# Kernel optimization log

Measured on AMD Instinct MI355X. Metric: run time of the kernel, lower is better.

The kernel has to match this reference:

```python
import math
from itertools import combinations
import jax, jax.numpy as jnp
import numpy as np

SEQ_LEN = 8
D_IN = 2048
D_OUT = 1152
TSS = 3          # temporal_set_size
WAY = 5
SHOT = 5
N_SUPPORT = WAY * SHOT
N_Q = 100
PE_SCALE = 0.1
LN_EPS = 1e-5

TUPLES = np.array(list(combinations(range(SEQ_LEN), TSS)), dtype=np.int32)  # [56, 3]
T_LEN = TUPLES.shape[0]  # 56


def _positional_encoding(seq_len, d):
    pos = np.arange(seq_len, dtype=np.float32)[:, None]
    div = np.exp(np.arange(0, d, 2, dtype=np.float32) * -(math.log(10000.0) / d))
    pe = np.zeros((seq_len, d), dtype=np.float32)
    pe[:, 0::2] = np.sin(pos * div) * PE_SCALE
    pe[:, 1::2] = np.cos(pos * div) * PE_SCALE
    return jnp.asarray(pe)


def _layernorm(x, g, b):
    mu = jnp.mean(x, axis=-1, keepdims=True)
    var = jnp.mean((x - mu) ** 2, axis=-1, keepdims=True)
    return (x - mu) * jax.lax.rsqrt(var + LN_EPS) * g + b


def setup_inputs() -> dict:
    key = jax.random.key(0)
    ks = jax.random.split(key, 6)
    support_set = jax.random.normal(ks[0], (N_SUPPORT, SEQ_LEN, D_IN), dtype=jnp.float32)
    queries = jax.random.normal(ks[1], (N_Q, SEQ_LEN, D_IN), dtype=jnp.float32)
    # sorted episode layout: class c occupies rows [c*SHOT, (c+1)*SHOT)
    support_labels = jnp.repeat(jnp.arange(WAY, dtype=jnp.int64), SHOT)
    d_flat = TSS * D_IN  # 6144
    k_w = jax.random.normal(ks[2], (d_flat, D_OUT), dtype=jnp.float32) * 0.02
    k_b = jnp.zeros((D_OUT,), dtype=jnp.float32)
    v_w = jax.random.normal(ks[3], (d_flat, D_OUT), dtype=jnp.float32) * 0.02
    v_b = jnp.zeros((D_OUT,), dtype=jnp.float32)
    ln_g = jnp.ones((D_OUT,), dtype=jnp.float32)
    ln_b = jnp.zeros((D_OUT,), dtype=jnp.float32)
    return {"support_set": support_set, "queries": queries,
            "support_labels": support_labels,
            "k_w": k_w, "k_b": k_b, "v_w": v_w, "v_b": v_b,
            "ln_g": ln_g, "ln_b": ln_b}


def reference(support_set, queries, support_labels, k_w, k_b, v_w, v_b, ln_g, ln_b):
    pe = _positional_encoding(SEQ_LEN, D_IN)  # dropout is identity in eval mode
    s = support_set + pe
    q = queries + pe

    def tuplify(x):  # [N, S, D] -> [N, T_LEN, TSS*D]
        return x[:, TUPLES, :].reshape(x.shape[0], T_LEN, TSS * D_IN)

    s_t = tuplify(s)
    q_t = tuplify(q)

    sk = _layernorm(s_t @ k_w + k_b, ln_g, ln_b)  # [25, 56, 1152]
    qk = _layernorm(q_t @ k_w + k_b, ln_g, ln_b)  # [100, 56, 1152]
    sv = s_t @ v_w + v_b                           # [25, 56, 1152]
    qv = q_t @ v_w + v_b                           # [100, 56, 1152]

    scale = 1.0 / math.sqrt(D_OUT)
    dists = []
    align = None
    for c in range(WAY):  # fixed small class loop; class rows are a static slice
        class_k = sk[c * SHOT:(c + 1) * SHOT]  # [SHOT, 56, 1152]
        class_v = sv[c * SHOT:(c + 1) * SHOT]
        # scores: [Q, T, K, T] == torch permute(0,2,1,3) of [Q, K, T, T]
        scores = jnp.einsum('qtd,ksd->qtks', qk, class_k) * scale
        flat = scores.reshape(N_Q, T_LEN, SHOT * T_LEN)
        sm = jax.nn.softmax(flat, axis=-1)
        sm = sm.reshape(N_Q, T_LEN, SHOT, T_LEN).transpose(0, 2, 1, 3)  # [Q, K, T, T]
        align = sm.sum(axis=1)  # [Q, T, T]
        proto = jnp.einsum('qkts,ksd->qtd', sm, class_v)  # [Q, 56, 1152]
        diff = qv - proto
        dists.append(-jnp.sum(diff * diff, axis=(-2, -1)) / T_LEN)  # [Q]
    logits = jnp.stack(dists, axis=1)  # [Q, WAY]
    return logits, align
```

## Files before the change

kernel.cpp:

```cpp
#include <hip/hip_runtime.h>
#include <hip/hip_bf16.h>
#include <math.h>

#define SEQ_LEN 8
#define D_IN 2048
#define D_OUT 1152
#define WAY 5
#define SHOT 5
#define N_SUPPORT 25
#define N_Q 100
#define N_SEQ 125
#define N_ROWS 1000
#define T_LEN 56
#define KS_LEN 280
#define KS_PAD 288
#define NCOLS 6912
#define MQT 5600
#define DPC 9

typedef __attribute__((ext_vector_type(4))) float f32x4;
typedef __attribute__((ext_vector_type(8))) short bf16x8;

__constant__ int TUP[T_LEN][3] = {
  {0,1,2},{0,1,3},{0,1,4},{0,1,5},{0,1,6},{0,1,7},{0,2,3},{0,2,4},{0,2,5},{0,2,6},
  {0,2,7},{0,3,4},{0,3,5},{0,3,6},{0,3,7},{0,4,5},{0,4,6},{0,4,7},{0,5,6},{0,5,7},
  {0,6,7},{1,2,3},{1,2,4},{1,2,5},{1,2,6},{1,2,7},{1,3,4},{1,3,5},{1,3,6},{1,3,7},
  {1,4,5},{1,4,6},{1,4,7},{1,5,6},{1,5,7},{1,6,7},{2,3,4},{2,3,5},{2,3,6},{2,3,7},
  {2,4,5},{2,4,6},{2,4,7},{2,5,6},{2,5,7},{2,6,7},{3,4,5},{3,4,6},{3,4,7},{3,5,6},
  {3,5,7},{3,6,7},{4,5,6},{4,5,7},{4,6,7},{5,6,7}
};

__device__ __forceinline__ ushort f2bf(float f) {
  union { float f; unsigned u; } v; v.f = f;
  unsigned r = v.u + 0x7FFFu + ((v.u >> 16) & 1u);
  return (ushort)(r >> 16);
}
__device__ __forceinline__ float bf2f(ushort u) {
  union { unsigned u; float f; } v; v.u = ((unsigned)u) << 16;
  return v.f;
}
__device__ __forceinline__ void gload16(const void* g, const void* l) {
  __builtin_amdgcn_global_load_lds(
      (const __attribute__((address_space(1))) unsigned int*)g,
      (__attribute__((address_space(3))) unsigned int*)l, 16, 0, 0);
}
template<int N> __device__ __forceinline__ void vmw() {
  asm volatile("s_waitcnt vmcnt(%0)" :: "n"(N) : "memory");
}

__global__ __launch_bounds__(256) void pe_add(const float* __restrict__ sup,
                                              const float* __restrict__ que,
                                              ushort* __restrict__ X) {
  int idx = blockIdx.x * 256 + threadIdx.x;
  if (idx >= N_ROWS * D_IN) return;
  int d = idx & (D_IN - 1);
  int r = idx >> 11;
  int i = r & 7;
  int h2 = d & ~1;
  float freq = expf((float)h2 * (-9.210340371976184f / (float)D_IN));
  float ang = (float)i * freq;
  float pe = ((d & 1) ? cosf(ang) : sinf(ang)) * 0.1f;
  float src = (r < N_SUPPORT * SEQ_LEN) ? sup[idx] : que[idx - N_SUPPORT * SEQ_LEN * D_IN];
  X[idx] = f2bf(src + pe);
}

__global__ __launch_bounds__(256) void wtrans(const float* __restrict__ kw,
                                              const float* __restrict__ vw,
                                              ushort* __restrict__ WT) {
  __shared__ float tile[64][65];
  int bx = blockIdx.x;
  int by = blockIdx.y;
  int b = bx / 18;
  int n0 = (bx % 18) * 64;
  int k0 = by * 64;
  const float* src = ((b & 1) ? vw : kw) + (size_t)(b >> 1) * D_IN * D_OUT;
  int tid = threadIdx.x;
#pragma unroll
  for (int it = 0; it < 4; ++it) {
    int lin4 = it * 256 + tid;
    int kk = lin4 >> 4;
    int n4 = (lin4 & 15) * 4;
    float4 v = *(const float4*)(src + (size_t)(k0 + kk) * D_OUT + n0 + n4);
    tile[kk][n4 + 0] = v.x; tile[kk][n4 + 1] = v.y;
    tile[kk][n4 + 2] = v.z; tile[kk][n4 + 3] = v.w;
  }
  __syncthreads();
#pragma unroll
  for (int it = 0; it < 4; ++it) {
    int lin = it * 1024 + tid * 4;
    int nn = lin >> 6, kk = lin & 63;
    ushort4 o;
    o.x = f2bf(tile[kk + 0][nn]); o.y = f2bf(tile[kk + 1][nn]);
    o.z = f2bf(tile[kk + 2][nn]); o.w = f2bf(tile[kk + 3][nn]);
    *(ushort4*)&WT[((size_t)(b * D_OUT + n0 + nn)) * D_IN + k0 + kk] = o;
  }
}

template<int EPI, int NT>
__global__ __launch_bounds__(256) void gemm_bt(
    const ushort* __restrict__ A, const ushort* __restrict__ BT,
    float* __restrict__ C,
    int M, int N, int K, int lda, int ldb, int ldc, float alpha,
    long batchA, long batchB, long batchC) {
  constexpr int JF = NT / 32;
  constexpr int NCH = 8 + NT / 16;
  __shared__ ushort As[2][128][32];
  __shared__ ushort Bs[2][NT][32];
  int z = blockIdx.z;
  A  += (size_t)z * batchA;
  BT += (size_t)z * batchB;
  C  += (size_t)z * batchC;

  int tid = threadIdx.x;
  int wid = tid >> 6, lane = tid & 63;
  int l16 = lane & 15, lk = lane >> 4;
  int wr = wid >> 1, wc = wid & 1;
  int row0 = blockIdx.x * 128, col0 = blockIdx.y * NT;
  int lrow = lane >> 2;
  int lcol = ((lane & 3) ^ ((lane >> 3) & 3)) * 8;
  int rslot = (lk ^ ((l16 >> 1) & 3)) * 8;

  auto stage = [&](int buf, int t) {
    int k0 = t * 32;
    for (int c = wid; c < NCH; c += 4) {
      if (c < 8) {
        int grow = row0 + c * 16 + lrow;
        grow = grow < M ? grow : M - 1;
        gload16(A + (size_t)grow * lda + k0 + lcol, &As[buf][c * 16][0]);
      } else {
        int gcol = col0 + (c - 8) * 16 + lrow;
        gcol = gcol < N ? gcol : N - 1;
        gload16(BT + (size_t)gcol * ldb + k0 + lcol, &Bs[buf][(c - 8) * 16][0]);
      }
    }
  };

  f32x4 acc[4][JF] = {};
  int nk = K / 32;
  stage(0, 0);
  for (int t = 0; t < nk; ++t) {
    int cur = t & 1;
    if (t + 1 < nk) {
      stage(cur ^ 1, t + 1);
      if constexpr ((NCH & 3) == 0) {
        vmw<NCH / 4>();
      } else {
        if (wid < (NCH & 3)) vmw<NCH / 4 + 1>(); else vmw<NCH / 4>();
      }
    } else {
      vmw<0>();
    }
    __builtin_amdgcn_s_barrier();
    __builtin_amdgcn_sched_barrier(0);
    bf16x8 af[4], bv[JF];
#pragma unroll
    for (int m = 0; m < 4; ++m)
      af[m] = *(const bf16x8*)&As[cur][wr * 64 + m * 16 + l16][rslot];
#pragma unroll
    for (int j = 0; j < JF; ++j)
      bv[j] = *(const bf16x8*)&Bs[cur][wc * (NT / 2) + j * 16 + l16][rslot];
#pragma unroll
    for (int m = 0; m < 4; ++m)
#pragma unroll
      for (int j = 0; j < JF; ++j)
        acc[m][j] = __builtin_amdgcn_mfma_f32_16x16x32_bf16(af[m], bv[j], acc[m][j], 0, 0, 0);
    __builtin_amdgcn_sched_barrier(0);
    __builtin_amdgcn_s_barrier();
  }

#pragma unroll
  for (int m = 0; m < 4; ++m)
#pragma unroll
    for (int j = 0; j < JF; ++j) {
      int col = col0 + wc * (NT / 2) + j * 16 + l16;
#pragma unroll
      for (int r = 0; r < 4; ++r) {
        int row = row0 + wr * 64 + m * 16 + lk * 4 + r;
        if (row < M && col < N)
          C[(size_t)row * ldc + col] = (EPI == 1) ? acc[m][j][r] * alpha : acc[m][j][r];
      }
    }
}

__global__ __launch_bounds__(256) void pv_dist(const ushort* __restrict__ SM,
                                               const ushort* __restrict__ SVT,
                                               const ushort* __restrict__ QV,
                                               float* __restrict__ DP) {
  __shared__ ushort Bs[128][296];
  int tid = threadIdx.x, wid = tid >> 6, lane = tid & 63;
  int l16 = lane & 15, lk = lane >> 4;
  int row0 = blockIdx.x * 128, col0 = blockIdx.y * 128, c = blockIdx.z;
  const ushort* sm = SM + (size_t)c * MQT * KS_PAD;
  const ushort* bt = SVT + ((size_t)c * D_OUT + col0) * KS_PAD;
  {
    int r = tid >> 1, h = tid & 1;
    const ushort* srcr = bt + (size_t)r * KS_PAD + h * 144;
#pragma unroll
    for (int i = 0; i < 18; ++i) {
      uint4 v = *(const uint4*)(srcr + i * 8);
      *(uint4*)&Bs[r][h * 144 + i * 8] = v;
    }
  }
  __syncthreads();

  int ra0 = row0 + wid * 32 + l16;      if (ra0 > MQT - 1) ra0 = MQT - 1;
  int ra1 = row0 + wid * 32 + 16 + l16; if (ra1 > MQT - 1) ra1 = MQT - 1;
  const ushort* a0 = sm + (size_t)ra0 * KS_PAD + lk * 8;
  const ushort* a1 = sm + (size_t)ra1 * KS_PAD + lk * 8;

  f32x4 acc[2][8] = {};
#pragma unroll
  for (int ks = 0; ks < 9; ++ks) {
    bf16x8 af0 = *(const bf16x8*)(a0 + ks * 32);
    bf16x8 af1 = *(const bf16x8*)(a1 + ks * 32);
    bf16x8 bv[8];
#pragma unroll
    for (int j = 0; j < 8; ++j)
      bv[j] = *(const bf16x8*)&Bs[j * 16 + l16][ks * 32 + lk * 8];
#pragma unroll
    for (int j = 0; j < 8; ++j) {
      acc[0][j] = __builtin_amdgcn_mfma_f32_16x16x32_bf16(af0, bv[j], acc[0][j], 0, 0, 0);
      acc[1][j] = __builtin_amdgcn_mfma_f32_16x16x32_bf16(af1, bv[j], acc[1][j], 0, 0, 0);
    }
  }

  float sq[2][4] = {};
#pragma unroll
  for (int m = 0; m < 2; ++m)
#pragma unroll
    for (int r = 0; r < 4; ++r) {
      int row = row0 + wid * 32 + m * 16 + lk * 4 + r;
      int rowc = row < MQT ? row : MQT - 1;
      const ushort* qvr = QV + (size_t)rowc * D_OUT + col0;
#pragma unroll
      for (int j = 0; j < 8; ++j) {
        float qvv = bf2f(qvr[j * 16 + l16]);
        float d = qvv - acc[m][j][r];
        sq[m][r] += d * d;
      }
    }
#pragma unroll
  for (int m = 0; m < 2; ++m)
#pragma unroll
    for (int r = 0; r < 4; ++r) {
      sq[m][r] += __shfl_xor(sq[m][r], 1);
      sq[m][r] += __shfl_xor(sq[m][r], 2);
      sq[m][r] += __shfl_xor(sq[m][r], 4);
      sq[m][r] += __shfl_xor(sq[m][r], 8);
    }
  if (l16 == 0) {
    float* dp = DP + (size_t)c * MQT * DPC;
#pragma unroll
    for (int m = 0; m < 2; ++m)
#pragma unroll
      for (int r = 0; r < 4; ++r) {
        int row = row0 + wid * 32 + m * 16 + lk * 4 + r;
        if (row < MQT) dp[(size_t)row * DPC + blockIdx.y] = sq[m][r];
      }
  }
}

__global__ __launch_bounds__(256) void combine_ln(const float* __restrict__ G,
                                                  const float* __restrict__ kb,
                                                  const float* __restrict__ vb,
                                                  const float* __restrict__ lng,
                                                  const float* __restrict__ lnb,
                                                  ushort* __restrict__ skbf,
                                                  ushort* __restrict__ qkbf,
                                                  ushort* __restrict__ sv,
                                                  ushort* __restrict__ qvbf) {
  int gw = blockIdx.x * 4 + (threadIdx.x >> 6);
  int lane = threadIdx.x & 63;
  int t = gw % T_LEN, n = gw / T_LEN;
  const float* g0 = G + (size_t)(n * 8 + TUP[t][0]) * NCOLS;
  const float* g1 = G + (size_t)(n * 8 + TUP[t][1]) * NCOLS + 2 * D_OUT;
  const float* g2 = G + (size_t)(n * 8 + TUP[t][2]) * NCOLS + 4 * D_OUT;
  bool isq = (n >= N_SUPPORT);
  int c = n / SHOT, s = n % SHOT;
  ushort* vout = isq ? qvbf + ((size_t)(n - N_SUPPORT) * T_LEN + t) * D_OUT
                     : sv + ((size_t)c * KS_PAD + s * T_LEN + t) * D_OUT;
  ushort* kout = isq ? qkbf + ((size_t)(n - N_SUPPORT) * T_LEN + t) * D_OUT
                     : skbf + ((size_t)c * KS_PAD + s * T_LEN + t) * D_OUT;
  float kvx[9], kvy[9], s1 = 0.f, s2 = 0.f;
#pragma unroll
  for (int i = 0; i < 9; ++i) {
    int d = i * 128 + lane * 2;
    float2 a = *(const float2*)(g0 + d);
    float2 b = *(const float2*)(g0 + D_OUT + d);
    float2 c1 = *(const float2*)(g1 + d);
    float2 c2 = *(const float2*)(g1 + D_OUT + d);
    float2 e1 = *(const float2*)(g2 + d);
    float2 e2 = *(const float2*)(g2 + D_OUT + d);
    float2 kb2 = *(const float2*)(kb + d);
    float2 vb2 = *(const float2*)(vb + d);
    float kx = a.x + c1.x + e1.x + kb2.x;
    float ky = a.y + c1.y + e1.y + kb2.y;
    float vx = b.x + c2.x + e2.x + vb2.x;
    float vy = b.y + c2.y + e2.y + vb2.y;
    kvx[i] = kx; kvy[i] = ky;
    ushort2 vv; vv.x = f2bf(vx); vv.y = f2bf(vy);
    *(ushort2*)(vout + d) = vv;
    s1 += kx + ky;
    s2 += kx * kx + ky * ky;
  }
#pragma unroll
  for (int m = 32; m > 0; m >>= 1) {
    s1 += __shfl_xor(s1, m);
    s2 += __shfl_xor(s2, m);
  }
  float mu = s1 * (1.0f / D_OUT);
  float var = s2 * (1.0f / D_OUT) - mu * mu;
  float rs = rsqrtf(var + 1e-5f);
#pragma unroll
  for (int i = 0; i < 9; ++i) {
    int d = i * 128 + lane * 2;
    float2 g2v = *(const float2*)(lng + d);
    float2 b2v = *(const float2*)(lnb + d);
    ushort2 o;
    o.x = f2bf((kvx[i] - mu) * rs * g2v.x + b2v.x);
    o.y = f2bf((kvy[i] - mu) * rs * g2v.y + b2v.y);
    *(ushort2*)(kout + d) = o;
  }
}

__global__ __launch_bounds__(256) void svtrans(const ushort* __restrict__ sv,
                                               ushort* __restrict__ svT) {
  __shared__ ushort tile[32][65];
  int c = blockIdx.z;
  int d0 = blockIdx.x * 64;
  int k0 = blockIdx.y * 32;
  const ushort* src = sv + (size_t)c * KS_PAD * D_OUT;
  ushort* dst = svT + (size_t)c * D_OUT * KS_PAD;
  int tid = threadIdx.x;
#pragma unroll
  for (int it = 0; it < 8; ++it) {
    int lin = it * 256 + tid;
    int ks = k0 + (lin >> 6), d = d0 + (lin & 63);
    tile[lin >> 6][lin & 63] = (ks < KS_LEN) ? src[(size_t)ks * D_OUT + d] : (ushort)0;
  }
  __syncthreads();
#pragma unroll
  for (int it = 0; it < 8; ++it) {
    int lin = it * 256 + tid;
    int d = lin >> 5, ks = lin & 31;
    dst[(size_t)(d0 + d) * KS_PAD + k0 + ks] = tile[ks][d];
  }
}

__global__ __launch_bounds__(256) void softmax_align(const float* __restrict__ S,
                                                     ushort* __restrict__ sm,
                                                     float* __restrict__ align_out) {
  __shared__ float pl[4][KS_LEN];
  int wid = threadIdx.x >> 6, lane = threadIdx.x & 63;
  int row = blockIdx.x * 4 + wid;
  const float* src = S + (size_t)row * KS_PAD;
  float v[5];
  float mx = -1e30f;
#pragma unroll
  for (int j = 0; j < 5; ++j) {
    int ks = lane + j * 64;
    v[j] = (ks < KS_LEN) ? src[ks] : -1e30f;
    mx = fmaxf(mx, v[j]);
  }
#pragma unroll
  for (int m = 32; m > 0; m >>= 1) mx = fmaxf(mx, __shfl_xor(mx, m));
  float sum = 0.f;
  float p[5];
#pragma unroll
  for (int j = 0; j < 5; ++j) {
    int ks = lane + j * 64;
    p[j] = (ks < KS_LEN) ? expf(v[j] - mx) : 0.f;
    sum += p[j];
  }
#pragma unroll
  for (int m = 32; m > 0; m >>= 1) sum += __shfl_xor(sum, m);
  float inv = 1.0f / sum;
  ushort* dst = sm + (size_t)row * KS_PAD;
#pragma unroll
  for (int j = 0; j < 5; ++j) {
    int ks = lane + j * 64;
    if (ks < KS_PAD) dst[ks] = f2bf((ks < KS_LEN) ? p[j] * inv : 0.f);
  }
  int c = row / MQT;
  if (c == WAY - 1) {
#pragma unroll
    for (int j = 0; j < 5; ++j) {
      int ks = lane + j * 64;
      if (ks < KS_LEN) pl[wid][ks] = p[j] * inv;
    }
    __syncthreads();
    if (lane < T_LEN) {
      float a = 0.f;
#pragma unroll
      for (int k = 0; k < SHOT; ++k) a += pl[wid][k * T_LEN + lane];
      int qt = row - (WAY - 1) * MQT;
      align_out[(size_t)(qt / T_LEN) * (T_LEN * T_LEN) + (qt % T_LEN) * T_LEN + lane] = a;
    }
  }
}

__global__ __launch_bounds__(256) void logits_k(const float* __restrict__ DP,
                                                float* __restrict__ out) {
  __shared__ float red[256];
  int q = blockIdx.x / WAY, c = blockIdx.x % WAY;
  const float* base = DP + ((size_t)c * MQT + q * T_LEN) * DPC;
  int tid = threadIdx.x;
  float s = 0.f;
  for (int i = tid; i < T_LEN * DPC; i += 256) s += base[i];
  red[tid] = s;
  __syncthreads();
  for (int sft = 128; sft > 0; sft >>= 1) {
    if (tid < sft) red[tid] += red[tid + sft];
    __syncthreads();
  }
  if (tid == 0) out[blockIdx.x] = -red[0] * (1.0f / T_LEN);
}

extern "C" void kernel_launch(void* const* d_in, const int* in_sizes, int n_in,
                              void* d_out, int out_size, void* d_ws, size_t ws_size,
                              hipStream_t stream) {
  const float* sup  = (const float*)d_in[0];
  const float* que  = (const float*)d_in[1];
  const float* k_w  = (const float*)d_in[3];
  const float* k_b  = (const float*)d_in[4];
  const float* v_w  = (const float*)d_in[5];
  const float* v_b  = (const float*)d_in[6];
  const float* ln_g = (const float*)d_in[7];
  const float* ln_b = (const float*)d_in[8];
  float* out = (float*)d_out;

  char* w = (char*)d_ws;
  ushort* Xbf  = (ushort*)(w + 0);
  ushort* WT   = (ushort*)(w + 4096000);
  float*  G    = (float*)(w + 32407552);
  ushort* sv   = (ushort*)(w + 0);
  float*  S    = (float*)(w + 0);
  ushort* smbf = (ushort*)(w + 32407552);
  float*  DP   = (float*)(w + 0);
  ushort* qkbf = (ushort*)(w + 60055552);
  ushort* skbf = (ushort*)(w + 72957952);
  ushort* svT  = (ushort*)(w + 76275712);
  ushort* qvbf = (ushort*)(w + 79593472);

  const float scale = 0.02946278254943948f;

  pe_add<<<dim3(8000), 256, 0, stream>>>(sup, que, Xbf);
  wtrans<<<dim3(108, 32), 256, 0, stream>>>(k_w, v_w, WT);
  gemm_bt<0, 64><<<dim3(8, 108, 1), 256, 0, stream>>>(
      Xbf, WT, G,
      N_ROWS, NCOLS, D_IN, D_IN, D_IN, NCOLS, 1.0f, 0, 0, 0);
  combine_ln<<<dim3(1750), 256, 0, stream>>>(
      G, k_b, v_b, ln_g, ln_b, skbf, qkbf, sv, qvbf);
  svtrans<<<dim3(18, 9, WAY), 256, 0, stream>>>(sv, svT);
  gemm_bt<1, 96><<<dim3(44, 3, WAY), 256, 0, stream>>>(
      qkbf, skbf, S,
      MQT, KS_PAD, D_OUT, D_OUT, D_OUT, KS_PAD, scale,
      0, (long)KS_PAD * D_OUT, (long)MQT * KS_PAD);
  softmax_align<<<dim3(7000), 256, 0, stream>>>(S, smbf, out + N_Q * WAY);
  pv_dist<<<dim3(44, 9, WAY), 256, 0, stream>>>(smbf, svT, qvbf, DP);
  logits_k<<<dim3(N_Q * WAY), 256, 0, stream>>>(DP, out);
}
```

Before: 195.9 us.

## Add configurable multi-stage GEMM pipeline and XCD-aware block swizzling

Generalizes the bf16 GEMM's shared-memory pipeline from double buffering to a template depth, using three stages for the projection GEMM, with runtime vmcnt waits. Remaps flat block indices so that blocks sharing the same weight or B tile land on the same XCD, applied to the projection GEMM, the score GEMM and pv_dist. The goal is to hide more load latency and improve L2 reuse across chiplets. In exchange it uses more LDS per block, launches padded grids whose extra blocks exit early, and adds a runtime switch for the wait count.

```diff
diff --git a/kernel.cpp b/kernel.cpp
--- a/kernel.cpp
+++ b/kernel.cpp
@@ -47,6 +47,16 @@
 template<int N> __device__ __forceinline__ void vmw() {
   asm volatile("s_waitcnt vmcnt(%0)" :: "n"(N) : "memory");
 }
+__device__ __forceinline__ void vmw_rt(int n) {
+  switch (n) {
+    case 0: vmw<0>(); break;
+    case 3: vmw<3>(); break;
+    case 4: vmw<4>(); break;
+    case 6: vmw<6>(); break;
+    case 8: vmw<8>(); break;
+    default: vmw<0>(); break;
+  }
+}
 
 __global__ __launch_bounds__(256) void pe_add(const float* __restrict__ sup,
                                               const float* __restrict__ que,
@@ -96,7 +106,7 @@
   }
 }
 
-template<int EPI, int NT>
+template<int EPI, int NT, int DEPTH, int SWZ>
 __global__ __launch_bounds__(256) void gemm_bt(
     const ushort* __restrict__ A, const ushort* __restrict__ BT,
     float* __restrict__ C,
@@ -104,18 +114,31 @@
     long batchA, long batchB, long batchC) {
   constexpr int JF = NT / 32;
   constexpr int NCH = 8 + NT / 16;
-  __shared__ ushort As[2][128][32];
-  __shared__ ushort Bs[2][NT][32];
-  int z = blockIdx.z;
-  A  += (size_t)z * batchA;
-  BT += (size_t)z * batchB;
-  C  += (size_t)z * batchC;
+  __shared__ ushort As[DEPTH][128][32];
+  __shared__ ushort Bs[DEPTH][NT][32];
+
+  int bx, by, bz;
+  if constexpr (SWZ == 1) {
+    int L = blockIdx.x, xcd = L & 7, s = L >> 3;
+    by = (s >> 3) * 8 + xcd;
+    if (by >= 108) return;
+    bx = s & 7; bz = 0;
+  } else if constexpr (SWZ == 2) {
+    int L = blockIdx.x, xcd = L & 7, s = L >> 3;
+    bx = (s % 6) * 8 + xcd;
+    if (bx >= 44) return;
+    int g = s / 6; by = g % 3; bz = g / 3;
+  } else { bx = blockIdx.x; by = blockIdx.y; bz = blockIdx.z; }
+
+  A  += (size_t)bz * batchA;
+  BT += (size_t)bz * batchB;
+  C  += (size_t)bz * batchC;
 
   int tid = threadIdx.x;
   int wid = tid >> 6, lane = tid & 63;
   int l16 = lane & 15, lk = lane >> 4;
   int wr = wid >> 1, wc = wid & 1;
-  int row0 = blockIdx.x * 128, col0 = blockIdx.y * NT;
+  int row0 = bx * 128, col0 = by * NT;
   int lrow = lane >> 2;
   int lcol = ((lane & 3) ^ ((lane >> 3) & 3)) * 8;
   int rslot = (lk ^ ((l16 >> 1) & 3)) * 8;
@@ -135,21 +158,18 @@
     }
   };
 
+  int perw = NCH / 4 + ((wid < (NCH & 3)) ? 1 : 0);
   f32x4 acc[4][JF] = {};
   int nk = K / 32;
-  stage(0, 0);
+#pragma unroll
+  for (int i = 0; i < DEPTH - 1; ++i)
+    if (i < nk) stage(i, i);
   for (int t = 0; t < nk; ++t) {
-    int cur = t & 1;
-    if (t + 1 < nk) {
-      stage(cur ^ 1, t + 1);
-      if constexpr ((NCH & 3) == 0) {
-        vmw<NCH / 4>();
-      } else {
-        if (wid < (NCH & 3)) vmw<NCH / 4 + 1>(); else vmw<NCH / 4>();
-      }
-    } else {
-      vmw<0>();
-    }
+    int cur = t % DEPTH;
+    int ts = t + DEPTH - 1;
+    if (ts < nk) stage(ts % DEPTH, ts);
+    int rem = nk - 1 - t; if (rem > DEPTH - 1) rem = DEPTH - 1;
+    vmw_rt(rem * perw);
     __builtin_amdgcn_s_barrier();
     __builtin_amdgcn_sched_barrier(0);
     bf16x8 af[4], bv[JF];
@@ -187,9 +207,13 @@
                                                const ushort* __restrict__ QV,
                                                float* __restrict__ DP) {
   __shared__ ushort Bs[128][296];
+  int L = blockIdx.x, xcd = L & 7, s = L >> 3;
+  int bx = (s % 6) * 8 + xcd;
+  if (bx >= 44) return;
+  int g = s / 6; int by = g % 9, bz = g / 9;
   int tid = threadIdx.x, wid = tid >> 6, lane = tid & 63;
   int l16 = lane & 15, lk = lane >> 4;
-  int row0 = blockIdx.x * 128, col0 = blockIdx.y * 128, c = blockIdx.z;
+  int row0 = bx * 128, col0 = by * 128, c = bz;
   const ushort* sm = SM + (size_t)c * MQT * KS_PAD;
   const ushort* bt = SVT + ((size_t)c * D_OUT + col0) * KS_PAD;
   {
@@ -255,7 +279,7 @@
 #pragma unroll
       for (int r = 0; r < 4; ++r) {
         int row = row0 + wid * 32 + m * 16 + lk * 4 + r;
-        if (row < MQT) dp[(size_t)row * DPC + blockIdx.y] = sq[m][r];
+        if (row < MQT) dp[(size_t)row * DPC + by] = sq[m][r];
       }
   }
 }
@@ -446,17 +470,17 @@
 
   pe_add<<<dim3(8000), 256, 0, stream>>>(sup, que, Xbf);
   wtrans<<<dim3(108, 32), 256, 0, stream>>>(k_w, v_w, WT);
-  gemm_bt<0, 64><<<dim3(8, 108, 1), 256, 0, stream>>>(
+  gemm_bt<0, 64, 3, 1><<<dim3(896), 256, 0, stream>>>(
       Xbf, WT, G,
       N_ROWS, NCOLS, D_IN, D_IN, D_IN, NCOLS, 1.0f, 0, 0, 0);
   combine_ln<<<dim3(1750), 256, 0, stream>>>(
       G, k_b, v_b, ln_g, ln_b, skbf, qkbf, sv, qvbf);
   svtrans<<<dim3(18, 9, WAY), 256, 0, stream>>>(sv, svT);
-  gemm_bt<1, 96><<<dim3(44, 3, WAY), 256, 0, stream>>>(
+  gemm_bt<1, 96, 2, 2><<<dim3(720), 256, 0, stream>>>(
       qkbf, skbf, S,
       MQT, KS_PAD, D_OUT, D_OUT, D_OUT, KS_PAD, scale,
       0, (long)KS_PAD * D_OUT, (long)MQT * KS_PAD);
   softmax_align<<<dim3(7000), 256, 0, stream>>>(S, smbf, out + N_Q * WAY);
-  pv_dist<<<dim3(44, 9, WAY), 256, 0, stream>>>(smbf, svT, qvbf, DP);
+  pv_dist<<<dim3(2160), 256, 0, stream>>>(smbf, svT, qvbf, DP);
   logits_k<<<dim3(N_Q * WAY), 256, 0, stream>>>(DP, out);
 }
```

Result: no change. 194.5 us (-0.7%).
